# Optimization experiments

Measured on AMD Instinct MI355X. Metric: run time of the kernel, lower is better.

The kernel has to match this reference:

```python
import jax, jax.numpy as jnp
import numpy as np

N_NODES = 100000
N_EDGES = 1600000
D_IN = 128
D_HID = 128
D_OUT = 2
N_GRAPHS = 64


def setup_inputs() -> dict:
    key = jax.random.key(0)
    ks = jax.random.split(key, 10)
    x = jax.random.normal(ks[0], (N_NODES, D_IN), dtype=jnp.float32)
    edge_index = jax.random.randint(ks[1], (2, N_EDGES), 0, N_NODES, dtype=jnp.int64)
    batch = jnp.sort(jax.random.randint(ks[2], (N_NODES,), 0, N_GRAPHS, dtype=jnp.int64))
    s_in = 1.0 / np.sqrt(D_IN)
    s_hid = 1.0 / np.sqrt(D_HID)
    W1 = jax.random.uniform(ks[3], (D_IN, D_HID), jnp.float32, -s_in, s_in)
    b1 = jnp.zeros((D_HID,), jnp.float32)
    W2 = jax.random.uniform(ks[4], (D_HID, D_HID), jnp.float32, -s_hid, s_hid)
    b2 = jnp.zeros((D_HID,), jnp.float32)
    W3 = jax.random.uniform(ks[5], (D_HID, D_OUT), jnp.float32, -s_hid, s_hid)
    b3 = jnp.zeros((D_OUT,), jnp.float32)
    return {"x": x, "edge_index": edge_index, "batch": batch,
            "W1": W1, "b1": b1, "W2": W2, "b2": b2, "W3": W3, "b3": b3}


def gcn_conv(x, W, b, src, dst, num_nodes):
    # PyG GCNConv: x' = D^{-1/2} (A + I) D^{-1/2} X W + b, edges flow src -> dst
    h = x @ W  # [N, F] transform first (smaller feature dim path)
    ones = jnp.ones((src.shape[0],), h.dtype)
    deg = jax.ops.segment_sum(ones, dst, num_segments=num_nodes) + 1.0  # self-loop
    dinv = jax.lax.rsqrt(deg)
    norm = dinv[src] * dinv[dst]  # per-edge symmetric normalization
    agg = jax.ops.segment_sum(h[src] * norm[:, None], dst, num_segments=num_nodes)
    out = agg + h * (dinv * dinv)[:, None]  # self-loop contribution
    return out + b


def reference(x, edge_index, batch, W1, b1, W2, b2, W3, b3):
    src, dst = edge_index[0], edge_index[1]
    n = x.shape[0]
    h = jax.nn.relu(gcn_conv(x, W1, b1, src, dst, n))   # dropout is identity in eval
    h = jax.nn.relu(gcn_conv(h, W2, b2, src, dst, n))
    h = gcn_conv(h, W3, b3, src, dst, n)
    # global mean pool over batch segments
    sums = jax.ops.segment_sum(h, batch, num_segments=N_GRAPHS)
    cnts = jax.ops.segment_sum(jnp.ones((n,), h.dtype), batch, num_segments=N_GRAPHS)
    return sums / jnp.maximum(cnts, 1.0)[:, None]
```

## Files before the change

kernel.cpp:

```cpp
#include <hip/hip_runtime.h>
#include <hip/hip_fp16.h>

#define EPB 8192
#define SEGCAP 12288

typedef __attribute__((ext_vector_type(8))) _Float16 half8;
typedef __attribute__((ext_vector_type(4))) float f32x4;


__global__ void scan1(const int* __restrict__ v, int* __restrict__ incl,
                      int* __restrict__ bsum, int n) {
    __shared__ int tmp[256];
    int t = threadIdx.x;
    int gid = blockIdx.x * 256 + t;
    tmp[t] = (gid < n) ? v[gid] : 0;
    __syncthreads();
    for (int off = 1; off < 256; off <<= 1) {
        int x = (t >= off) ? tmp[t - off] : 0;
        __syncthreads();
        tmp[t] += x;
        __syncthreads();
    }
    if (gid < n) incl[gid] = tmp[t];
    if (t == 255) bsum[blockIdx.x] = tmp[255];
}

__global__ void scan2(const int* __restrict__ bsum, int* __restrict__ boff, int nb) {
    __shared__ int tmp[512];
    int t = threadIdx.x;
    int orig = (t < nb) ? bsum[t] : 0;
    tmp[t] = orig;
    __syncthreads();
    for (int off = 1; off < 512; off <<= 1) {
        int x = (t >= off) ? tmp[t - off] : 0;
        __syncthreads();
        tmp[t] += x;
        __syncthreads();
    }
    if (t < nb) boff[t] = tmp[t] - orig;
}

__global__ void basec_k(const int* __restrict__ incl, const int* __restrict__ boff,
                        const int* __restrict__ hist, int* __restrict__ base, int T) {
    int i = blockIdx.x * 256 + threadIdx.x;
    if (i < T) base[i] = incl[i] + boff[blockIdx.x] - hist[i];
}


__global__ __launch_bounds__(256) void hist_k(const int* __restrict__ dst,
                                              int* __restrict__ hist,
                                              int E, int nblk, int nbuk) {
    __shared__ int h[512];
    int t = threadIdx.x;
    for (int i = t; i < nbuk; i += 256) h[i] = 0;
    __syncthreads();
    int start = blockIdx.x * EPB;
    int end = start + EPB; if (end > E) end = E;
    for (int e = start + t; e < end; e += 256) atomicAdd(&h[dst[e] >> 8], 1);
    __syncthreads();
    for (int i = t; i < nbuk; i += 256) hist[i * nblk + blockIdx.x] = h[i];
}


__global__ __launch_bounds__(256) void binscatter_k(const int* __restrict__ src,
                                                    const int* __restrict__ dst,
                                                    const int* __restrict__ base,
                                                    unsigned int* __restrict__ binned,
                                                    int E, int nblk, int nbuk) {
    __shared__ int hloc[512];
    __shared__ int lstart[512];
    __shared__ int stmp[512];
    __shared__ unsigned int pk[EPB];
    __shared__ unsigned short bid[EPB];
    int t = threadIdx.x;
    int blk = blockIdx.x;
    int start = blk * EPB;
    int end = start + EPB; if (end > E) end = E;
    int cntE = end - start;

    for (int i = t; i < nbuk; i += 256) hloc[i] = 0;
    __syncthreads();
    for (int e = start + t; e < end; e += 256) atomicAdd(&hloc[dst[e] >> 8], 1);
    __syncthreads();
    for (int i = t; i < 512; i += 256) stmp[i] = (i < nbuk) ? hloc[i] : 0;
    __syncthreads();
    for (int off = 1; off < 512; off <<= 1) {
        int v0 = (t >= off) ? stmp[t - off] : 0;
        int v1 = stmp[t + 256 - off];
        __syncthreads();
        stmp[t] += v0;
        stmp[t + 256] += v1;
        __syncthreads();
    }
    for (int i = t; i < nbuk; i += 256) {
        int ex = stmp[i] - hloc[i];
        lstart[i] = ex;
        hloc[i] = ex;
    }
    __syncthreads();
    for (int e = start + t; e < end; e += 256) {
        int d = dst[e];
        int b = d >> 8;
        int r = atomicAdd(&hloc[b], 1);
        pk[r] = (unsigned int)src[e] | ((unsigned int)(d & 255) << 24);
        bid[r] = (unsigned short)b;
    }
    __syncthreads();
    for (int i = t; i < cntE; i += 256) {
        int b = bid[i];
        binned[base[b * nblk + blk] + (i - lstart[b])] = pk[i];
    }
}


__global__ __launch_bounds__(256) void group_k(const unsigned int* __restrict__ binned,
                                               const int* __restrict__ base,
                                               int* __restrict__ rowptr,
                                               float* __restrict__ dinv,
                                               int* __restrict__ col,
                                               int nblk, int nbuk, int N, int E) {
    __shared__ int cntL[256];
    __shared__ int sc[256];
    __shared__ int cur[256];
    __shared__ int stage[SEGCAP];
    int b = blockIdx.x, t = threadIdx.x;
    int segstart = base[b * nblk];
    int segend = (b + 1 < nbuk) ? base[(b + 1) * nblk] : E;
    int seglen = segend - segstart;

    cntL[t] = 0;
    __syncthreads();
    for (int i = segstart + t; i < segend; i += 256)
        atomicAdd(&cntL[binned[i] >> 24], 1);
    __syncthreads();
    sc[t] = cntL[t];
    __syncthreads();
    for (int off = 1; off < 256; off <<= 1) {
        int v = (t >= off) ? sc[t - off] : 0;
        __syncthreads();
        sc[t] += v;
        __syncthreads();
    }
    int n = (b << 8) + t;
    if (n < N) {
        rowptr[n + 1] = segstart + sc[t];
        dinv[n] = rsqrtf((float)cntL[t] + 1.0f);
    }
    if (b == 0 && t == 0) rowptr[0] = 0;
    cur[t] = sc[t] - cntL[t];
    __syncthreads();
    if (seglen <= SEGCAP) {
        for (int i = segstart + t; i < segend; i += 256) {
            unsigned int p = binned[i];
            int r = atomicAdd(&cur[p >> 24], 1);
            stage[r] = (int)(p & 0xFFFFFFu);
        }
        __syncthreads();
        for (int i = t; i < seglen; i += 256) col[segstart + i] = stage[i];
    } else {
        for (int i = segstart + t; i < segend; i += 256) {
            unsigned int p = binned[i];
            int r = atomicAdd(&cur[p >> 24], 1);
            col[segstart + r] = (int)(p & 0xFFFFFFu);
        }
    }
}


__global__ __launch_bounds__(256) void packW_k(const float* __restrict__ W,
                                               _Float16* __restrict__ Wp) {
    int t = blockIdx.x * 256 + threadIdx.x;
    int lane = t & 63, qct = t >> 6;
    int q = qct >> 3, ct = qct & 7;
    int krow = q * 32 + (lane >> 4) * 8;
    int c = ct * 16 + (lane & 15);
#pragma unroll
    for (int j = 0; j < 8; ++j)
        Wp[(size_t)t * 8 + j] = (_Float16)W[(krow + j) * 128 + c];
}


template<typename XT>
__global__ __launch_bounds__(256) void gemm_mfma(const XT* __restrict__ X,
                                                 const _Float16* __restrict__ Wp,
                                                 const float* __restrict__ dinv,
                                                 _Float16* __restrict__ Gh, int M) {
    constexpr bool F32 = (sizeof(XT) == 4);
    __shared__ _Float16 Wl[16384];
    int t = threadIdx.x;
    for (int i = t; i < 2048; i += 256)
        *(float4*)&Wl[(size_t)i * 8] = ((const float4*)Wp)[i];

    int wid = t >> 6, lane = t & 63;
    int row0 = blockIdx.x * 64 + wid * 16;
    int arow = row0 + (lane & 15); if (arow >= M) arow = M - 1;
    int kgrp = (lane >> 4) * 8;

    half8 a[4];
    if constexpr (F32) {
#pragma unroll
        for (int q = 0; q < 4; ++q) {
            const float* p = (const float*)X + (size_t)arow * 128 + q * 32 + kgrp;
            float4 u = *(const float4*)p;
            float4 v = *(const float4*)(p + 4);
            half8 h;
            h[0] = (_Float16)u.x; h[1] = (_Float16)u.y;
            h[2] = (_Float16)u.z; h[3] = (_Float16)u.w;
            h[4] = (_Float16)v.x; h[5] = (_Float16)v.y;
            h[6] = (_Float16)v.z; h[7] = (_Float16)v.w;
            a[q] = h;
        }
    } else {
#pragma unroll
        for (int q = 0; q < 4; ++q)
            a[q] = *(const half8*)((const _Float16*)X + (size_t)arow * 128 + q * 32 + kgrp);
    }
    __syncthreads();

    f32x4 acc[8];
#pragma unroll
    for (int ct = 0; ct < 8; ++ct) acc[ct] = (f32x4){0.f, 0.f, 0.f, 0.f};

#pragma unroll
    for (int q = 0; q < 4; ++q) {
#pragma unroll
        for (int ct = 0; ct < 8; ++ct) {
            half8 b = *(const half8*)&Wl[(size_t)((q * 8 + ct) * 64 + lane) * 8];
            acc[ct] = __builtin_amdgcn_mfma_f32_16x16x32_f16(a[q], b, acc[ct], 0, 0, 0);
        }
    }

    int rbase = row0 + (lane >> 4) * 4;
#pragma unroll
    for (int reg = 0; reg < 4; ++reg) {
        int r = rbase + reg;
        if (r < M) {
            float di = dinv[r];
#pragma unroll
            for (int ct = 0; ct < 8; ++ct)
                Gh[(size_t)r * 128 + ct * 16 + (lane & 15)] = (_Float16)(acc[ct][reg] * di);
        }
    }
}


__device__ __forceinline__ void addpk(__half2* acc, float4 v) {
    const __half2* h = reinterpret_cast<const __half2*>(&v);
#pragma unroll
    for (int j = 0; j < 4; ++j) acc[j] = __hadd2(acc[j], h[j]);
}

__global__ __launch_bounds__(256) void aggregate128h(const float4* __restrict__ G4,
                                                     const float* __restrict__ dinv,
                                                     const int* __restrict__ rowptr,
                                                     const int* __restrict__ col,
                                                     const float4* __restrict__ bias4,
                                                     float4* __restrict__ OutH,
                                                     int relu, int N) {
    int n = blockIdx.x * 4 + (threadIdx.x >> 6);
    if (n >= N) return;
    int lane = threadIdx.x & 63;
    int f = lane & 15;
    int slot = lane >> 4;
    int e0 = rowptr[n], e1 = rowptr[n + 1];
    __half2 acc[4];
#pragma unroll
    for (int j = 0; j < 4; ++j) acc[j] = __float2half2_rn(0.f);

    int base = e0;
    for (; base + 16 <= e1; base += 16) {
        int s0 = col[base + slot];
        int s1 = col[base + 4 + slot];
        int s2 = col[base + 8 + slot];
        int s3 = col[base + 12 + slot];
        float4 v0 = G4[s0 * 16 + f];
        float4 v1 = G4[s1 * 16 + f];
        float4 v2 = G4[s2 * 16 + f];
        float4 v3 = G4[s3 * 16 + f];
        addpk(acc, v0); addpk(acc, v1); addpk(acc, v2); addpk(acc, v3);
    }
    for (int idx = base + slot; idx < e1; idx += 4) {
        float4 v = G4[col[idx] * 16 + f];
        addpk(acc, v);
    }
    float a[8];
#pragma unroll
    for (int j = 0; j < 4; ++j) {
        float2 fp = __half22float2(acc[j]);
        a[2 * j] = fp.x;
        a[2 * j + 1] = fp.y;
    }
#pragma unroll
    for (int j = 0; j < 8; ++j) {
        a[j] += __shfl_xor(a[j], 16);
        a[j] += __shfl_xor(a[j], 32);
    }
    if (slot == 0) {
        float4 g = G4[n * 16 + f];
        float s[8];
        {
            const __half2* h = reinterpret_cast<const __half2*>(&g);
#pragma unroll
            for (int j = 0; j < 4; ++j) {
                float2 fp = __half22float2(h[j]);
                s[2 * j] = fp.x;
                s[2 * j + 1] = fp.y;
            }
        }
        float di = dinv[n];
        float4 b0 = bias4[f * 2], b1 = bias4[f * 2 + 1];
        float o[8];
        o[0] = di * (a[0] + s[0]) + b0.x;
        o[1] = di * (a[1] + s[1]) + b0.y;
        o[2] = di * (a[2] + s[2]) + b0.z;
        o[3] = di * (a[3] + s[3]) + b0.w;
        o[4] = di * (a[4] + s[4]) + b1.x;
        o[5] = di * (a[5] + s[5]) + b1.y;
        o[6] = di * (a[6] + s[6]) + b1.z;
        o[7] = di * (a[7] + s[7]) + b1.w;
        if (relu) {
#pragma unroll
            for (int j = 0; j < 8; ++j) o[j] = fmaxf(o[j], 0.f);
        }
        __half2 hh[4];
#pragma unroll
        for (int j = 0; j < 4; ++j) hh[j] = __floats2half2_rn(o[2 * j], o[2 * j + 1]);
        OutH[n * 16 + f] = *(float4*)hh;
    }
}


__global__ __launch_bounds__(256) void gemm_out2h(const __half2* __restrict__ Xh,
                                                  const float* __restrict__ W3,
                                                  const float* __restrict__ dinv,
                                                  float* __restrict__ G3, int M) {
    int gtid = blockIdx.x * blockDim.x + threadIdx.x;
    int row = gtid >> 6;
    int lane = threadIdx.x & 63;
    if (row >= M) return;
    __half2 h = Xh[(size_t)row * 64 + lane];
    float2 f = __half22float2(h);
    int c = lane * 2;
    float a0 = f.x * W3[c * 2 + 0] + f.y * W3[(c + 1) * 2 + 0];
    float a1 = f.x * W3[c * 2 + 1] + f.y * W3[(c + 1) * 2 + 1];
    for (int off = 32; off; off >>= 1) {
        a0 += __shfl_down(a0, off);
        a1 += __shfl_down(a1, off);
    }
    if (lane == 0) {
        float di = dinv[row];
        G3[(size_t)row * 2 + 0] = a0 * di;
        G3[(size_t)row * 2 + 1] = a1 * di;
    }
}


__global__ void aggregate2(const float2* __restrict__ G3, const float* __restrict__ dinv,
                           const int* __restrict__ rowptr, const int* __restrict__ col,
                           const float* __restrict__ b3,
                           float2* __restrict__ O3, int N) {
    int n = blockIdx.x * blockDim.x + threadIdx.x;
    if (n >= N) return;
    float s0 = 0.f, s1 = 0.f;
    int e0 = rowptr[n], e1 = rowptr[n + 1];
    int e = e0;
    for (; e + 4 <= e1; e += 4) {
        float2 v0 = G3[col[e]];
        float2 v1 = G3[col[e + 1]];
        float2 v2 = G3[col[e + 2]];
        float2 v3 = G3[col[e + 3]];
        s0 += v0.x + v1.x + v2.x + v3.x;
        s1 += v0.y + v1.y + v2.y + v3.y;
    }
    for (; e < e1; ++e) {
        float2 v = G3[col[e]];
        s0 += v.x; s1 += v.y;
    }
    float2 g = G3[n];
    float di = dinv[n];
    float2 o;
    o.x = di * (s0 + g.x) + b3[0];
    o.y = di * (s1 + g.y) + b3[1];
    O3[n] = o;
}


__global__ void pool_k(const float* __restrict__ O3, const int* __restrict__ batch,
                       float* __restrict__ pool, int N) {
    __shared__ float ls[64 * 3];
    for (int i = threadIdx.x; i < 192; i += blockDim.x) ls[i] = 0.f;
    __syncthreads();
    int n = blockIdx.x * blockDim.x + threadIdx.x;
    if (n < N) {
        int g = batch[n];
        atomicAdd(&ls[g * 3 + 0], O3[(size_t)n * 2 + 0]);
        atomicAdd(&ls[g * 3 + 1], O3[(size_t)n * 2 + 1]);
        atomicAdd(&ls[g * 3 + 2], 1.0f);
    }
    __syncthreads();
    for (int i = threadIdx.x; i < 192; i += blockDim.x)
        if (ls[i] != 0.f) atomicAdd(&pool[i], ls[i]);
}

__global__ void finalize_k(const float* __restrict__ pool, float* __restrict__ out) {
    int t = threadIdx.x;
    if (t < 128) {
        int g = t >> 1, c = t & 1;
        out[t] = pool[g * 3 + c] / fmaxf(pool[g * 3 + 2], 1.0f);
    }
}


extern "C" void kernel_launch(void* const* d_in, const int* in_sizes, int n_in,
                              void* d_out, int out_size, void* d_ws, size_t ws_size,
                              hipStream_t stream) {
    const float* x   = (const float*)d_in[0];
    const int*  edge = (const int*)d_in[1];
    const int*  batch= (const int*)d_in[2];
    const float* W1  = (const float*)d_in[3];
    const float* b1  = (const float*)d_in[4];
    const float* W2  = (const float*)d_in[5];
    const float* b2  = (const float*)d_in[6];
    const float* W3  = (const float*)d_in[7];
    const float* b3  = (const float*)d_in[8];
    float* out = (float*)d_out;

    int N = in_sizes[0] / 128;
    int E = in_sizes[1] / 2;
    const int* src = edge;
    const int* dst = edge + E;

    int nblk1 = (E + EPB - 1) / EPB;
    int nbuk  = (N + 255) >> 8;
    int T     = nbuk * nblk1;
    int nb2   = (T + 255) / 256;

    char* base_ws = (char*)d_ws;
    size_t off = 0;
    auto alloc = [&](size_t bytes) -> void* {
        void* r = base_ws + off;
        off = (off + bytes + 255) & ~(size_t)255;
        return r;
    };
    _Float16*     GhA    = (_Float16*)alloc((size_t)N * 128 * 2);
    _Float16*     GhB    = (_Float16*)alloc((size_t)N * 128 * 2);
    _Float16*     Wp1    = (_Float16*)alloc(16384 * 2);
    _Float16*     Wp2    = (_Float16*)alloc(16384 * 2);
    float*        dinv   = (float*)alloc((size_t)N * 4);
    int*          rowptr = (int*)alloc((size_t)(N + 1) * 4);
    int*          col    = (int*)alloc((size_t)E * 4);
    unsigned int* binned = (unsigned int*)alloc((size_t)E * 4);
    int*          hist   = (int*)alloc((size_t)T * 4);
    int*          incl   = (int*)alloc((size_t)T * 4);
    int*          bsum   = (int*)alloc(1024 * 4);
    int*          boff   = (int*)alloc(1024 * 4);
    int*          basea  = (int*)alloc((size_t)(T + 1) * 4);
    float*        g3     = (float*)alloc((size_t)N * 2 * 4);
    float*        h3b    = (float*)alloc((size_t)N * 2 * 4);
    float*        pool   = (float*)alloc(64 * 3 * 4);

    hipMemsetAsync(pool, 0, 64 * 3 * 4, stream);

    packW_k<<<8, 256, 0, stream>>>(W1, Wp1);
    packW_k<<<8, 256, 0, stream>>>(W2, Wp2);

    hist_k<<<nblk1, 256, 0, stream>>>(dst, hist, E, nblk1, nbuk);
    scan1<<<nb2, 256, 0, stream>>>(hist, incl, bsum, T);
    scan2<<<1, 512, 0, stream>>>(bsum, boff, nb2);
    basec_k<<<nb2, 256, 0, stream>>>(incl, boff, hist, basea, T);
    binscatter_k<<<nblk1, 256, 0, stream>>>(src, dst, basea, binned, E, nblk1, nbuk);
    group_k<<<nbuk, 256, 0, stream>>>(binned, basea, rowptr, dinv, col, nblk1, nbuk, N, E);

    int gb = (N + 63) / 64;
    int ab = (N + 3) / 4;

    gemm_mfma<float><<<gb, 256, 0, stream>>>(x, Wp1, dinv, GhA, N);
    aggregate128h<<<ab, 256, 0, stream>>>((const float4*)GhA, dinv, rowptr, col,
                                          (const float4*)b1, (float4*)GhB, 1, N);
    gemm_mfma<_Float16><<<gb, 256, 0, stream>>>(GhB, Wp2, dinv, GhA, N);
    aggregate128h<<<ab, 256, 0, stream>>>((const float4*)GhA, dinv, rowptr, col,
                                          (const float4*)b2, (float4*)GhB, 1, N);
    gemm_out2h<<<(N * 64 + 255) / 256, 256, 0, stream>>>((const __half2*)GhB, W3, dinv, g3, N);
    aggregate2<<<(N + 255) / 256, 256, 0, stream>>>((const float2*)g3, dinv, rowptr, col,
                                                    b3, (float2*)h3b, N);
    pool_k<<<(N + 255) / 256, 256, 0, stream>>>(h3b, batch, pool, N);
    finalize_k<<<1, 128, 0, stream>>>(pool, out);
}
```

Before: 257.3 us.

## Shard hidden features into column slices and aggregate per slice

The hidden activations move from a row-major [N,128] fp16 layout to 8 column shards of [N,16] fp16. The GEMM kernels read and write this sharded layout, and a new aggregation kernel assigns each block one shard. Each shard (about 3.2 MB) is small enough that the random neighbor gathers can stay in cache, with 8 threads per node accumulating in fp32. The cost is that every edge's column index is now read 8 times instead of once, and each gathered access shrinks to 4 bytes.

```diff
diff --git a/kernel.cpp b/kernel.cpp
--- a/kernel.cpp
+++ b/kernel.cpp
@@ -186,6 +186,7 @@
                                                  const float* __restrict__ dinv,
                                                  _Float16* __restrict__ Gh, int M) {
     constexpr bool F32 = (sizeof(XT) == 4);
+    const size_t sstride = (size_t)M * 16;
     __shared__ _Float16 Wl[16384];
     int t = threadIdx.x;
     for (int i = t; i < 2048; i += 256)
@@ -211,9 +212,14 @@
             a[q] = h;
         }
     } else {
-#pragma unroll
-        for (int q = 0; q < 4; ++q)
-            a[q] = *(const half8*)((const _Float16*)X + (size_t)arow * 128 + q * 32 + kgrp);
+        int coff = lane >> 5;
+        int off = ((lane >> 4) & 1) * 8;
+#pragma unroll
+        for (int q = 0; q < 4; ++q) {
+            const _Float16* p = (const _Float16*)X +
+                (size_t)(2 * q + coff) * sstride + (size_t)arow * 16 + off;
+            a[q] = *(const half8*)p;
+        }
     }
     __syncthreads();
 
@@ -238,99 +244,60 @@
             float di = dinv[r];
 #pragma unroll
             for (int ct = 0; ct < 8; ++ct)
-                Gh[(size_t)r * 128 + ct * 16 + (lane & 15)] = (_Float16)(acc[ct][reg] * di);
-        }
-    }
-}
-
-
-__device__ __forceinline__ void addpk(__half2* acc, float4 v) {
-    const __half2* h = reinterpret_cast<const __half2*>(&v);
-#pragma unroll
-    for (int j = 0; j < 4; ++j) acc[j] = __hadd2(acc[j], h[j]);
-}
-
-__global__ __launch_bounds__(256) void aggregate128h(const float4* __restrict__ G4,
-                                                     const float* __restrict__ dinv,
-                                                     const int* __restrict__ rowptr,
-                                                     const int* __restrict__ col,
-                                                     const float4* __restrict__ bias4,
-                                                     float4* __restrict__ OutH,
-                                                     int relu, int N) {
-    int n = blockIdx.x * 4 + (threadIdx.x >> 6);
+                Gh[(size_t)ct * sstride + (size_t)r * 16 + (lane & 15)] =
+                    (_Float16)(acc[ct][reg] * di);
+        }
+    }
+}
+
+
+__global__ __launch_bounds__(256) void aggregate_shard(const _Float16* __restrict__ G,
+                                                       const float* __restrict__ dinv,
+                                                       const int* __restrict__ rowptr,
+                                                       const int* __restrict__ col,
+                                                       const float* __restrict__ bias,
+                                                       _Float16* __restrict__ Out,
+                                                       int relu, int N) {
+    int c = blockIdx.x & 7;
+    int g = blockIdx.x >> 3;
+    int slot = threadIdx.x >> 3;
+    int j = threadIdx.x & 7;
+    int n = g * 32 + slot;
     if (n >= N) return;
-    int lane = threadIdx.x & 63;
-    int f = lane & 15;
-    int slot = lane >> 4;
-    int e0 = rowptr[n], e1 = rowptr[n + 1];
-    __half2 acc[4];
-#pragma unroll
-    for (int j = 0; j < 4; ++j) acc[j] = __float2half2_rn(0.f);
-
-    int base = e0;
-    for (; base + 16 <= e1; base += 16) {
-        int s0 = col[base + slot];
-        int s1 = col[base + 4 + slot];
-        int s2 = col[base + 8 + slot];
-        int s3 = col[base + 12 + slot];
-        float4 v0 = G4[s0 * 16 + f];
-        float4 v1 = G4[s1 * 16 + f];
-        float4 v2 = G4[s2 * 16 + f];
-        float4 v3 = G4[s3 * 16 + f];
-        addpk(acc, v0); addpk(acc, v1); addpk(acc, v2); addpk(acc, v3);
-    }
-    for (int idx = base + slot; idx < e1; idx += 4) {
-        float4 v = G4[col[idx] * 16 + f];
-        addpk(acc, v);
-    }
-    float a[8];
-#pragma unroll
-    for (int j = 0; j < 4; ++j) {
-        float2 fp = __half22float2(acc[j]);
-        a[2 * j] = fp.x;
-        a[2 * j + 1] = fp.y;
-    }
-#pragma unroll
-    for (int j = 0; j < 8; ++j) {
-        a[j] += __shfl_xor(a[j], 16);
-        a[j] += __shfl_xor(a[j], 32);
-    }
-    if (slot == 0) {
-        float4 g = G4[n * 16 + f];
-        float s[8];
-        {
-            const __half2* h = reinterpret_cast<const __half2*>(&g);
-#pragma unroll
-            for (int j = 0; j < 4; ++j) {
-                float2 fp = __half22float2(h[j]);
-                s[2 * j] = fp.x;
-                s[2 * j + 1] = fp.y;
-            }
-        }
-        float di = dinv[n];
-        float4 b0 = bias4[f * 2], b1 = bias4[f * 2 + 1];
-        float o[8];
-        o[0] = di * (a[0] + s[0]) + b0.x;
-        o[1] = di * (a[1] + s[1]) + b0.y;
-        o[2] = di * (a[2] + s[2]) + b0.z;
-        o[3] = di * (a[3] + s[3]) + b0.w;
-        o[4] = di * (a[4] + s[4]) + b1.x;
-        o[5] = di * (a[5] + s[5]) + b1.y;
-        o[6] = di * (a[6] + s[6]) + b1.z;
-        o[7] = di * (a[7] + s[7]) + b1.w;
-        if (relu) {
-#pragma unroll
-            for (int j = 0; j < 8; ++j) o[j] = fmaxf(o[j], 0.f);
-        }
-        __half2 hh[4];
-#pragma unroll
-        for (int j = 0; j < 4; ++j) hh[j] = __floats2half2_rn(o[2 * j], o[2 * j + 1]);
-        OutH[n * 16 + f] = *(float4*)hh;
-    }
-}
-
-
-__global__ __launch_bounds__(256) void gemm_out2h(const __half2* __restrict__ Xh,
+    const __half2* Gc = (const __half2*)(G + (size_t)c * N * 16);
+
+    int e0 = __builtin_nontemporal_load(&rowptr[n]);
+    int e1 = __builtin_nontemporal_load(&rowptr[n + 1]);
+    float ax = 0.f, ay = 0.f;
+    int e = e0;
+    for (; e + 4 <= e1; e += 4) {
+        int s0 = __builtin_nontemporal_load(&col[e]);
+        int s1 = __builtin_nontemporal_load(&col[e + 1]);
+        int s2 = __builtin_nontemporal_load(&col[e + 2]);
+        int s3 = __builtin_nontemporal_load(&col[e + 3]);
+        float2 f0 = __half22float2(Gc[(size_t)s0 * 8 + j]);
+        float2 f1 = __half22float2(Gc[(size_t)s1 * 8 + j]);
+        float2 f2 = __half22float2(Gc[(size_t)s2 * 8 + j]);
+        float2 f3 = __half22float2(Gc[(size_t)s3 * 8 + j]);
+        ax += f0.x + f1.x + f2.x + f3.x;
+        ay += f0.y + f1.y + f2.y + f3.y;
+    }
+    for (; e < e1; ++e) {
+        int s = __builtin_nontemporal_load(&col[e]);
+        float2 f = __half22float2(Gc[(size_t)s * 8 + j]);
+        ax += f.x; ay += f.y;
+    }
+    float2 sf = __half22float2(Gc[(size_t)n * 8 + j]);
+    float di = dinv[n];
+    float ox = di * (ax + sf.x) + bias[c * 16 + 2 * j];
+    float oy = di * (ay + sf.y) + bias[c * 16 + 2 * j + 1];
+    if (relu) { ox = fmaxf(ox, 0.f); oy = fmaxf(oy, 0.f); }
+    __half2 ho = __floats2half2_rn(ox, oy);
+    ((__half2*)(Out + (size_t)c * N * 16))[(size_t)n * 8 + j] = ho;
+}
+
+
+__global__ __launch_bounds__(256) void gemm_out2h(const _Float16* __restrict__ Xh,
                                                   const float* __restrict__ W3,
                                                   const float* __restrict__ dinv,
                                                   float* __restrict__ G3, int M) {
@@ -338,11 +305,12 @@
     int row = gtid >> 6;
     int lane = threadIdx.x & 63;
     if (row >= M) return;
-    __half2 h = Xh[(size_t)row * 64 + lane];
+    int c = lane >> 3, j = lane & 7;
+    __half2 h = ((const __half2*)(Xh + (size_t)c * M * 16))[(size_t)row * 8 + j];
     float2 f = __half22float2(h);
-    int c = lane * 2;
-    float a0 = f.x * W3[c * 2 + 0] + f.y * W3[(c + 1) * 2 + 0];
-    float a1 = f.x * W3[c * 2 + 1] + f.y * W3[(c + 1) * 2 + 1];
+    int fc = lane * 2;
+    float a0 = f.x * W3[fc * 2 + 0] + f.y * W3[(fc + 1) * 2 + 0];
+    float a1 = f.x * W3[fc * 2 + 1] + f.y * W3[(fc + 1) * 2 + 1];
     for (int off = 32; off; off >>= 1) {
         a0 += __shfl_down(a0, off);
         a1 += __shfl_down(a1, off);
@@ -472,15 +440,13 @@
     group_k<<<nbuk, 256, 0, stream>>>(binned, basea, rowptr, dinv, col, nblk1, nbuk, N, E);
 
     int gb = (N + 63) / 64;
-    int ab = (N + 3) / 4;
+    int ashard = ((N + 31) / 32) * 8;
 
     gemm_mfma<float><<<gb, 256, 0, stream>>>(x, Wp1, dinv, GhA, N);
-    aggregate128h<<<ab, 256, 0, stream>>>((const float4*)GhA, dinv, rowptr, col,
-                                          (const float4*)b1, (float4*)GhB, 1, N);
+    aggregate_shard<<<ashard, 256, 0, stream>>>(GhA, dinv, rowptr, col, b1, GhB, 1, N);
     gemm_mfma<_Float16><<<gb, 256, 0, stream>>>(GhB, Wp2, dinv, GhA, N);
-    aggregate128h<<<ab, 256, 0, stream>>>((const float4*)GhA, dinv, rowptr, col,
-                                          (const float4*)b2, (float4*)GhB, 1, N);
-    gemm_out2h<<<(N * 64 + 255) / 256, 256, 0, stream>>>((const __half2*)GhB, W3, dinv, g3, N);
+    aggregate_shard<<<ashard, 256, 0, stream>>>(GhA, dinv, rowptr, col, b2, GhB, 1, N);
+    gemm_out2h<<<(N * 64 + 255) / 256, 256, 0, stream>>>(GhB, W3, dinv, g3, N);
     aggregate2<<<(N + 255) / 256, 256, 0, stream>>>((const float2*)g3, dinv, rowptr, col,
                                                     b3, (float2*)h3b, N);
     pool_k<<<(N + 255) / 256, 256, 0, stream>>>(h3b, batch, pool, N);
```

Measured after the change: 423.2 us. 64.5% more time.

## Fuse layer-3 projection into aggregation and aggregation into pooling; vectorize histogram

Applied to the files above, without the earlier changes.

The second 128-wide aggregation now applies bias, ReLU and the 128x2 W3 projection in registers and writes only the scaled 2-wide result. This removes the fp16 hidden-state write and its re-read by a separate projection kernel. The final 2-wide aggregation is merged with mean pooling, which drops an intermediate buffer and a launch. The histogram kernel also loads dst as int4 vectors for full blocks. In exchange there are extra shuffle reductions and W3 loads per node, and the projection result now comes from fp32 values rather than fp16-rounded ones.

```diff
diff --git a/kernel.cpp b/kernel.cpp
--- a/kernel.cpp
+++ b/kernel.cpp
@@ -6,6 +6,7 @@
 
 typedef __attribute__((ext_vector_type(8))) _Float16 half8;
 typedef __attribute__((ext_vector_type(4))) float f32x4;
+typedef __attribute__((ext_vector_type(4))) int i32x4;
 
 
 __global__ void scan1(const int* __restrict__ v, int* __restrict__ incl,
@@ -56,7 +57,19 @@
     __syncthreads();
     int start = blockIdx.x * EPB;
     int end = start + EPB; if (end > E) end = E;
-    for (int e = start + t; e < end; e += 256) atomicAdd(&h[dst[e] >> 8], 1);
+    if (end - start == EPB) {
+        const i32x4* dv = (const i32x4*)(dst + start);
+#pragma unroll
+        for (int p = 0; p < 8; ++p) {
+            i32x4 d4 = dv[t + p * 256];
+            atomicAdd(&h[d4.x >> 8], 1);
+            atomicAdd(&h[d4.y >> 8], 1);
+            atomicAdd(&h[d4.z >> 8], 1);
+            atomicAdd(&h[d4.w >> 8], 1);
+        }
+    } else {
+        for (int e = start + t; e < end; e += 256) atomicAdd(&h[dst[e] >> 8], 1);
+    }
     __syncthreads();
     for (int i = t; i < nbuk; i += 256) hist[i * nblk + blockIdx.x] = h[i];
 }
@@ -255,8 +268,7 @@
                                                      const int* __restrict__ rowptr,
                                                      const int* __restrict__ col,
                                                      const float4* __restrict__ bias4,
-                                                     float4* __restrict__ OutH,
-                                                     int relu, int N) {
+                                                     float4* __restrict__ OutH, int N) {
     int n = blockIdx.x * 4 + (threadIdx.x >> 6);
     if (n >= N) return;
     int lane = threadIdx.x & 63;
@@ -273,14 +285,14 @@
         int s1 = col[base + 4 + slot];
         int s2 = col[base + 8 + slot];
         int s3 = col[base + 12 + slot];
-        float4 v0 = G4[s0 * 16 + f];
-        float4 v1 = G4[s1 * 16 + f];
-        float4 v2 = G4[s2 * 16 + f];
-        float4 v3 = G4[s3 * 16 + f];
+        float4 v0 = G4[(size_t)s0 * 16 + f];
+        float4 v1 = G4[(size_t)s1 * 16 + f];
+        float4 v2 = G4[(size_t)s2 * 16 + f];
+        float4 v3 = G4[(size_t)s3 * 16 + f];
         addpk(acc, v0); addpk(acc, v1); addpk(acc, v2); addpk(acc, v3);
     }
     for (int idx = base + slot; idx < e1; idx += 4) {
-        float4 v = G4[col[idx] * 16 + f];
+        float4 v = G4[(size_t)col[idx] * 16 + f];
         addpk(acc, v);
     }
     float a[8];
@@ -296,109 +308,152 @@
         a[j] += __shfl_xor(a[j], 32);
     }
     if (slot == 0) {
-        float4 g = G4[n * 16 + f];
-        float s[8];
-        {
-            const __half2* h = reinterpret_cast<const __half2*>(&g);
-#pragma unroll
-            for (int j = 0; j < 4; ++j) {
-                float2 fp = __half22float2(h[j]);
-                s[2 * j] = fp.x;
-                s[2 * j + 1] = fp.y;
-            }
-        }
+        float4 g = G4[(size_t)n * 16 + f];
+        const __half2* sp = (const __half2*)&g;
         float di = dinv[n];
         float4 b0 = bias4[f * 2], b1 = bias4[f * 2 + 1];
         float o[8];
-        o[0] = di * (a[0] + s[0]) + b0.x;
-        o[1] = di * (a[1] + s[1]) + b0.y;
-        o[2] = di * (a[2] + s[2]) + b0.z;
-        o[3] = di * (a[3] + s[3]) + b0.w;
-        o[4] = di * (a[4] + s[4]) + b1.x;
-        o[5] = di * (a[5] + s[5]) + b1.y;
-        o[6] = di * (a[6] + s[6]) + b1.z;
-        o[7] = di * (a[7] + s[7]) + b1.w;
-        if (relu) {
-#pragma unroll
-            for (int j = 0; j < 8; ++j) o[j] = fmaxf(o[j], 0.f);
-        }
+#pragma unroll
+        for (int j = 0; j < 4; ++j) {
+            float2 fp = __half22float2(sp[j]);
+            o[2 * j]     = di * (a[2 * j] + fp.x);
+            o[2 * j + 1] = di * (a[2 * j + 1] + fp.y);
+        }
+        o[0] += b0.x; o[1] += b0.y; o[2] += b0.z; o[3] += b0.w;
+        o[4] += b1.x; o[5] += b1.y; o[6] += b1.z; o[7] += b1.w;
+#pragma unroll
+        for (int j = 0; j < 8; ++j) o[j] = fmaxf(o[j], 0.f);
         __half2 hh[4];
 #pragma unroll
         for (int j = 0; j < 4; ++j) hh[j] = __floats2half2_rn(o[2 * j], o[2 * j + 1]);
-        OutH[n * 16 + f] = *(float4*)hh;
-    }
-}
-
-
-__global__ __launch_bounds__(256) void gemm_out2h(const __half2* __restrict__ Xh,
-                                                  const float* __restrict__ W3,
-                                                  const float* __restrict__ dinv,
-                                                  float* __restrict__ G3, int M) {
-    int gtid = blockIdx.x * blockDim.x + threadIdx.x;
-    int row = gtid >> 6;
+        OutH[(size_t)n * 16 + f] = *(float4*)hh;
+    }
+}
+
+
+__global__ __launch_bounds__(256) void aggregate128h_w3(const float4* __restrict__ G4,
+                                                        const float* __restrict__ dinv,
+                                                        const int* __restrict__ rowptr,
+                                                        const int* __restrict__ col,
+                                                        const float4* __restrict__ bias4,
+                                                        const float* __restrict__ W3,
+                                                        float* __restrict__ G3, int N) {
+    int n = blockIdx.x * 4 + (threadIdx.x >> 6);
+    if (n >= N) return;
     int lane = threadIdx.x & 63;
-    if (row >= M) return;
-    __half2 h = Xh[(size_t)row * 64 + lane];
-    float2 f = __half22float2(h);
-    int c = lane * 2;
-    float a0 = f.x * W3[c * 2 + 0] + f.y * W3[(c + 1) * 2 + 0];
-    float a1 = f.x * W3[c * 2 + 1] + f.y * W3[(c + 1) * 2 + 1];
-    for (int off = 32; off; off >>= 1) {
-        a0 += __shfl_down(a0, off);
-        a1 += __shfl_down(a1, off);
+    int f = lane & 15;
+    int slot = lane >> 4;
+    int e0 = rowptr[n], e1 = rowptr[n + 1];
+    __half2 acc[4];
+#pragma unroll
+    for (int j = 0; j < 4; ++j) acc[j] = __float2half2_rn(0.f);
+
+    int base = e0;
+    for (; base + 16 <= e1; base += 16) {
+        int s0 = col[base + slot];
+        int s1 = col[base + 4 + slot];
+        int s2 = col[base + 8 + slot];
+        int s3 = col[base + 12 + slot];
+        float4 v0 = G4[(size_t)s0 * 16 + f];
+        float4 v1 = G4[(size_t)s1 * 16 + f];
+        float4 v2 = G4[(size_t)s2 * 16 + f];
+        float4 v3 = G4[(size_t)s3 * 16 + f];
+        addpk(acc, v0); addpk(acc, v1); addpk(acc, v2); addpk(acc, v3);
+    }
+    for (int idx = base + slot; idx < e1; idx += 4) {
+        float4 v = G4[(size_t)col[idx] * 16 + f];
+        addpk(acc, v);
+    }
+    float a[8];
+#pragma unroll
+    for (int j = 0; j < 4; ++j) {
+        float2 fp = __half22float2(acc[j]);
+        a[2 * j] = fp.x;
+        a[2 * j + 1] = fp.y;
+    }
+#pragma unroll
+    for (int j = 0; j < 8; ++j) {
+        a[j] += __shfl_xor(a[j], 16);
+        a[j] += __shfl_xor(a[j], 32);
+    }
+    float p0 = 0.f, p1 = 0.f;
+    float di = dinv[n];
+    if (slot == 0) {
+        float4 g = G4[(size_t)n * 16 + f];
+        const __half2* sp = (const __half2*)&g;
+        float4 b0 = bias4[f * 2], b1 = bias4[f * 2 + 1];
+        float o[8];
+#pragma unroll
+        for (int j = 0; j < 4; ++j) {
+            float2 fp = __half22float2(sp[j]);
+            o[2 * j]     = di * (a[2 * j] + fp.x);
+            o[2 * j + 1] = di * (a[2 * j + 1] + fp.y);
+        }
+        o[0] += b0.x; o[1] += b0.y; o[2] += b0.z; o[3] += b0.w;
+        o[4] += b1.x; o[5] += b1.y; o[6] += b1.z; o[7] += b1.w;
+#pragma unroll
+        for (int j = 0; j < 8; ++j) o[j] = fmaxf(o[j], 0.f);
+        float w[16];
+        *(float4*)&w[0]  = ((const float4*)W3)[f * 4 + 0];
+        *(float4*)&w[4]  = ((const float4*)W3)[f * 4 + 1];
+        *(float4*)&w[8]  = ((const float4*)W3)[f * 4 + 2];
+        *(float4*)&w[12] = ((const float4*)W3)[f * 4 + 3];
+#pragma unroll
+        for (int j = 0; j < 8; ++j) {
+            p0 += o[j] * w[2 * j];
+            p1 += o[j] * w[2 * j + 1];
+        }
+    }
+#pragma unroll
+    for (int m = 1; m < 16; m <<= 1) {
+        p0 += __shfl_xor(p0, m);
+        p1 += __shfl_xor(p1, m);
     }
     if (lane == 0) {
-        float di = dinv[row];
-        G3[(size_t)row * 2 + 0] = a0 * di;
-        G3[(size_t)row * 2 + 1] = a1 * di;
-    }
-}
-
-
-__global__ void aggregate2(const float2* __restrict__ G3, const float* __restrict__ dinv,
-                           const int* __restrict__ rowptr, const int* __restrict__ col,
-                           const float* __restrict__ b3,
-                           float2* __restrict__ O3, int N) {
-    int n = blockIdx.x * blockDim.x + threadIdx.x;
-    if (n >= N) return;
-    float s0 = 0.f, s1 = 0.f;
-    int e0 = rowptr[n], e1 = rowptr[n + 1];
-    int e = e0;
-    for (; e + 4 <= e1; e += 4) {
-        float2 v0 = G3[col[e]];
-        float2 v1 = G3[col[e + 1]];
-        float2 v2 = G3[col[e + 2]];
-        float2 v3 = G3[col[e + 3]];
-        s0 += v0.x + v1.x + v2.x + v3.x;
-        s1 += v0.y + v1.y + v2.y + v3.y;
-    }
-    for (; e < e1; ++e) {
-        float2 v = G3[col[e]];
-        s0 += v.x; s1 += v.y;
-    }
-    float2 g = G3[n];
-    float di = dinv[n];
-    float2 o;
-    o.x = di * (s0 + g.x) + b3[0];
-    o.y = di * (s1 + g.y) + b3[1];
-    O3[n] = o;
-}
-
-
-__global__ void pool_k(const float* __restrict__ O3, const int* __restrict__ batch,
-                       float* __restrict__ pool, int N) {
-    __shared__ float ls[64 * 3];
-    for (int i = threadIdx.x; i < 192; i += blockDim.x) ls[i] = 0.f;
-    __syncthreads();
-    int n = blockIdx.x * blockDim.x + threadIdx.x;
+        G3[(size_t)n * 2 + 0] = p0 * di;
+        G3[(size_t)n * 2 + 1] = p1 * di;
+    }
+}
+
+
+__global__ __launch_bounds__(256) void agg2pool(const float2* __restrict__ G3,
+                                                const float* __restrict__ dinv,
+                                                const int* __restrict__ rowptr,
+                                                const int* __restrict__ col,
+                                                const float* __restrict__ b3,
+                                                const int* __restrict__ batch,
+                                                float* __restrict__ pool, int N) {
+    __shared__ float ls[192];
+    for (int i = threadIdx.x; i < 192; i += 256) ls[i] = 0.f;
+    __syncthreads();
+    int n = blockIdx.x * 256 + threadIdx.x;
     if (n < N) {
-        int g = batch[n];
-        atomicAdd(&ls[g * 3 + 0], O3[(size_t)n * 2 + 0]);
-        atomicAdd(&ls[g * 3 + 1], O3[(size_t)n * 2 + 1]);
-        atomicAdd(&ls[g * 3 + 2], 1.0f);
-    }
-    __syncthreads();
-    for (int i = threadIdx.x; i < 192; i += blockDim.x)
+        float s0 = 0.f, s1 = 0.f;
+        int e0 = rowptr[n], e1 = rowptr[n + 1];
+        int e = e0;
+        for (; e + 4 <= e1; e += 4) {
+            float2 v0 = G3[col[e]];
+            float2 v1 = G3[col[e + 1]];
+            float2 v2 = G3[col[e + 2]];
+            float2 v3 = G3[col[e + 3]];
+            s0 += v0.x + v1.x + v2.x + v3.x;
+            s1 += v0.y + v1.y + v2.y + v3.y;
+        }
+        for (; e < e1; ++e) {
+            float2 v = G3[col[e]];
+            s0 += v.x; s1 += v.y;
+        }
+        float2 g = G3[n];
+        float di = dinv[n];
+        float o0 = di * (s0 + g.x) + b3[0];
+        float o1 = di * (s1 + g.y) + b3[1];
+        int gb = batch[n];
+        atomicAdd(&ls[gb * 3 + 0], o0);
+        atomicAdd(&ls[gb * 3 + 1], o1);
+        atomicAdd(&ls[gb * 3 + 2], 1.0f);
+    }
+    __syncthreads();
+    for (int i = threadIdx.x; i < 192; i += 256)
         if (ls[i] != 0.f) atomicAdd(&pool[i], ls[i]);
 }
 
@@ -456,7 +511,6 @@
     int*          boff   = (int*)alloc(1024 * 4);
     int*          basea  = (int*)alloc((size_t)(T + 1) * 4);
     float*        g3     = (float*)alloc((size_t)N * 2 * 4);
-    float*        h3b    = (float*)alloc((size_t)N * 2 * 4);
     float*        pool   = (float*)alloc(64 * 3 * 4);
 
     hipMemsetAsync(pool, 0, 64 * 3 * 4, stream);
@@ -476,13 +530,11 @@
 
     gemm_mfma<float><<<gb, 256, 0, stream>>>(x, Wp1, dinv, GhA, N);
     aggregate128h<<<ab, 256, 0, stream>>>((const float4*)GhA, dinv, rowptr, col,
-                                          (const float4*)b1, (float4*)GhB, 1, N);
+                                          (const float4*)b1, (float4*)GhB, N);
     gemm_mfma<_Float16><<<gb, 256, 0, stream>>>(GhB, Wp2, dinv, GhA, N);
-    aggregate128h<<<ab, 256, 0, stream>>>((const float4*)GhA, dinv, rowptr, col,
-                                          (const float4*)b2, (float4*)GhB, 1, N);
-    gemm_out2h<<<(N * 64 + 255) / 256, 256, 0, stream>>>((const __half2*)GhB, W3, dinv, g3, N);
-    aggregate2<<<(N + 255) / 256, 256, 0, stream>>>((const float2*)g3, dinv, rowptr, col,
-                                                    b3, (float2*)h3b, N);
-    pool_k<<<(N + 255) / 256, 256, 0, stream>>>(h3b, batch, pool, N);
+    aggregate128h_w3<<<ab, 256, 0, stream>>>((const float4*)GhA, dinv, rowptr, col,
+                                             (const float4*)b2, W3, g3, N);
+    agg2pool<<<(N + 255) / 256, 256, 0, stream>>>((const float2*)g3, dinv, rowptr, col,
+                                                  b3, batch, pool, N);
     finalize_k<<<1, 128, 0, stream>>>(pool, out);
 }
```

Measured after the change: 233.0 us. -9.4%, faster.
